# Performance work log

Hardware: AMD Instinct MI355X
Metric: run time of the kernel (lower is better)

## Reference

```python
import jax, jax.numpy as jnp
import numpy as np

MARGIN = 0.3
IN_FEATURES = 128
NUM_CLASSES = 100
BATCH = 4096


def setup_inputs() -> dict:
    key = jax.random.key(0)
    k1, k2, k3, k4 = jax.random.split(key, 4)
    embeddings = jax.random.normal(k1, (BATCH, IN_FEATURES), dtype=jnp.float32)
    labels = jax.random.randint(k2, (BATCH,), 0, NUM_CLASSES, dtype=jnp.int64)
    # nn.Linear params (kaiming-uniform-ish scale)
    bound = 1.0 / np.sqrt(IN_FEATURES)
    fc_w = jax.random.uniform(k3, (NUM_CLASSES, IN_FEATURES), jnp.float32, -bound, bound)
    fc_b = jax.random.uniform(k4, (NUM_CLASSES,), jnp.float32, -bound, bound)
    return {"embeddings": embeddings, "labels": labels, "fc_w": fc_w, "fc_b": fc_b}


def _triplet_hard(emb, labels, margin):
    # pairwise squared euclidean distances: ||a||^2 + ||b||^2 - 2 a.b
    sq = jnp.sum(emb * emb, axis=1)  # [B]
    d2 = sq[:, None] + sq[None, :] - 2.0 * (emb @ emb.T)
    dist = jnp.sqrt(jnp.clip(d2, 1e-12))  # [B, B]
    same = labels[:, None] == labels[None, :]  # [B, B] (diag True, as in torch)
    neg_inf = jnp.float32(-jnp.inf)
    pos_inf = jnp.float32(jnp.inf)
    ap = jnp.max(jnp.where(same, dist, neg_inf), axis=1)  # hardest positive
    an = jnp.min(jnp.where(same, pos_inf, dist), axis=1)  # hardest negative
    # MarginRankingLoss(target=1): mean(relu(-(an - ap) + margin))
    return jnp.mean(jax.nn.relu(ap - an + margin))


def _cross_entropy(logits, labels):
    logp = jax.nn.log_softmax(logits, axis=-1)
    return -jnp.mean(jnp.take_along_axis(logp, labels[:, None], axis=1)[:, 0])


def reference(embeddings, labels, fc_w, fc_b):
    logits = embeddings @ fc_w.T + fc_b  # [B, C]
    triplet = _triplet_hard(embeddings, labels, MARGIN)
    ce = _cross_entropy(logits, labels)
    return triplet + ce
```

## Files before the change

### kernel.cpp

```cpp
#include <hip/hip_runtime.h>
#include <math.h>

#define BATCH 4096
#define DIM 128
#define NCLS 100
#define MARGIN 0.3f
#define NTILE 544
#define GRID_MAIN 800

typedef __attribute__((ext_vector_type(8))) short short8;
typedef __attribute__((ext_vector_type(4))) float f32x4;

__device__ __forceinline__ unsigned short f2bf(float f) {
    unsigned int u = __float_as_uint(f);
    unsigned int r = (u + 0x7FFFu + ((u >> 16) & 1u)) >> 16;
    return (unsigned short)r;
}
__device__ __forceinline__ float bf2f(unsigned short b) {
    return __uint_as_float(((unsigned int)b) << 16);
}

#define ENC_MAX_ID 0x80000000u
#define ENC_MIN_ID 0x403FFFFFu
__device__ __forceinline__ unsigned int enc_max(float v) {
    return (__float_as_uint(v) >> 1) | 0x80000000u;
}
__device__ __forceinline__ float dec_max(unsigned int k) {
    return __uint_as_float((k & 0x7FFFFFFFu) << 1);
}
__device__ __forceinline__ unsigned int enc_min(float v) {
    return 0x7FFFFFFFu - (__float_as_uint(v) >> 1);
}
__device__ __forceinline__ float dec_min(unsigned int k) {
    return __uint_as_float((0x7FFFFFFFu - k) << 1);
}


__global__ __launch_bounds__(256) void prep_kernel(
        const float* __restrict__ emb, const float* __restrict__ fcw,
        unsigned short* __restrict__ ebf, float* __restrict__ sq,
        unsigned short* __restrict__ wbf, unsigned int* __restrict__ fanz) {
    int bid = blockIdx.x, tid = threadIdx.x;
    if (bid < 256) {
        int wave = tid >> 6, lane = tid & 63;
        unsigned int* dstg = reinterpret_cast<unsigned int*>(ebf) + bid * 1024;
        #pragma unroll
        for (int r = 0; r < 4; ++r) {
            int rowl = wave * 4 + r;
            int row = bid * 16 + rowl;
            const float2* src = reinterpret_cast<const float2*>(emb + row * DIM);
            float2 xy = src[lane];
            unsigned short b0 = f2bf(xy.x), b1 = f2bf(xy.y);
            float y0 = bf2f(b0), y1 = bf2f(b1);
            dstg[(lane >> 2) * 64 + rowl * 4 + (lane & 3)] =
                ((unsigned int)b1 << 16) | (unsigned int)b0;
            float acc = y0 * y0 + y1 * y1;
            #pragma unroll
            for (int off = 1; off < 64; off <<= 1) acc += __shfl_xor(acc, off, 64);
            if (lane == 0) sq[row] = acc;
        }
    } else {
        int idx = (bid - 256) * 256 + tid;
        for (int k = idx; k < 112 * DIM; k += 512) {
            int cls = k >> 7, d = k & 127;
            int dst = (cls >> 4) * 2048 + (d >> 3) * 128 + (cls & 15) * 8 + (d & 7);
            wbf[dst] = (k < NCLS * DIM) ? f2bf(fcw[k]) : (unsigned short)0;
        }
        for (int w = idx; w < 8194; w += 512)
            fanz[w] = 0;
    }
}

__global__ __launch_bounds__(256) void main_kernel(
        const unsigned short* __restrict__ ebf, const unsigned short* __restrict__ wbf,
        const float* __restrict__ sq, const int* __restrict__ labels,
        const float* __restrict__ fcb,
        unsigned int* __restrict__ maxk, unsigned int* __restrict__ mink,
        float* __restrict__ ce_sum, int* __restrict__ ticket,
        float* __restrict__ out) {
    __shared__ float lg[16][128];
    __shared__ unsigned int colk[512];
    __shared__ int lastFlag;
    int bid = blockIdx.x, tid = threadIdx.x;
    int wave = tid >> 6, lane = tid & 63;
    int lm = lane & 15, lq = lane >> 4;

    if (bid < NTILE) {
        int q = 0, rem = bid;
        while (rem >= 4 * (16 - q)) { rem -= 4 * (16 - q); ++q; }
        int cpr = 16 - q;
        int sub = rem / cpr, coff = rem % cpr;
        int rowgrp = 4 * q + sub;
        int chunk  = q + coff;

        int rbase = rowgrp * 64 + wave * 16;
        const unsigned short* apt = ebf + (rbase >> 4) * 2048 + lane * 8;
        short8 a0 = *reinterpret_cast<const short8*>(apt);
        short8 a1 = *reinterpret_cast<const short8*>(apt + 512);
        short8 a2 = *reinterpret_cast<const short8*>(apt + 1024);
        short8 a3 = *reinterpret_cast<const short8*>(apt + 1536);

        int labr[4];
        float sqr[4];
        #pragma unroll
        for (int r = 0; r < 4; ++r) {
            labr[r] = labels[rbase + lq * 4 + r];
            sqr[r]  = sq[rbase + lq * 4 + r];
        }

        colk[tid] = 0; colk[256 + tid] = 0;
        __syncthreads();

        float rmax[4] = {-INFINITY, -INFINITY, -INFINITY, -INFINITY};
        float rmin[4] = { INFINITY,  INFINITY,  INFINITY,  INFINITY};

        int cbase = chunk * 256;
        const unsigned short* bbase = ebf + (cbase >> 4) * 2048 + lane * 8;
        #pragma unroll 2
        for (int ct = 0; ct < 16; ++ct) {
            int col = cbase + ct * 16 + lm;
            const unsigned short* bp = bbase + ct * 2048;
            short8 b0 = *reinterpret_cast<const short8*>(bp);
            short8 b1 = *reinterpret_cast<const short8*>(bp + 512);
            short8 b2 = *reinterpret_cast<const short8*>(bp + 1024);
            short8 b3 = *reinterpret_cast<const short8*>(bp + 1536);
            f32x4 c = {0.f, 0.f, 0.f, 0.f};
            c = __builtin_amdgcn_mfma_f32_16x16x32_bf16(a0, b0, c, 0, 0, 0);
            c = __builtin_amdgcn_mfma_f32_16x16x32_bf16(a1, b1, c, 0, 0, 0);
            c = __builtin_amdgcn_mfma_f32_16x16x32_bf16(a2, b2, c, 0, 0, 0);
            c = __builtin_amdgcn_mfma_f32_16x16x32_bf16(a3, b3, c, 0, 0, 0);
            float sqc = sq[col];
            int lc = labels[col];
            float cmax = -INFINITY, cmin = INFINITY;
            #pragma unroll
            for (int r = 0; r < 4; ++r) {
                float v = fmaxf(fmaf(c[r], -2.0f, sqc) + sqr[r], 0.f);
                bool same = (lc == labr[r]);
                rmax[r] = same ? fmaxf(rmax[r], v) : rmax[r];
                rmin[r] = same ? rmin[r] : fminf(rmin[r], v);
                cmax    = same ? fmaxf(cmax, v) : cmax;
                cmin    = same ? cmin : fminf(cmin, v);
            }
            cmax = fmaxf(cmax, __shfl_xor(cmax, 16, 64));
            cmax = fmaxf(cmax, __shfl_xor(cmax, 32, 64));
            cmin = fminf(cmin, __shfl_xor(cmin, 16, 64));
            cmin = fminf(cmin, __shfl_xor(cmin, 32, 64));
            if (lq == 0) {
                atomicMax(&colk[ct * 16 + lm], enc_max(fmaxf(cmax, 0.f)));
                atomicMax(&colk[256 + ct * 16 + lm], enc_min(fmaxf(cmin, 0.f)));
            }
        }
        #pragma unroll
        for (int off = 1; off < 16; off <<= 1) {
            #pragma unroll
            for (int r = 0; r < 4; ++r) {
                rmax[r] = fmaxf(rmax[r], __shfl_xor(rmax[r], off, 64));
                rmin[r] = fminf(rmin[r], __shfl_xor(rmin[r], off, 64));
            }
        }
        if (lm == 0) {
            int row0 = rbase + lq * 4;
            #pragma unroll
            for (int r = 0; r < 4; ++r) {
                unsigned int kx = enc_max(fmaxf(rmax[r], 0.f));
                unsigned int kn = enc_min(fmaxf(rmin[r], 0.f));
                if (kx != ENC_MAX_ID)
                    __hip_atomic_fetch_max(&maxk[row0 + r], kx,
                                           __ATOMIC_RELAXED, __HIP_MEMORY_SCOPE_AGENT);
                if (kn != ENC_MIN_ID)
                    __hip_atomic_fetch_max(&mink[row0 + r], kn,
                                           __ATOMIC_RELAXED, __HIP_MEMORY_SCOPE_AGENT);
            }
        }
        __syncthreads();
        {
            unsigned int kx = colk[tid], kn = colk[256 + tid];
            int col = cbase + tid;
            if (kx > ENC_MAX_ID)
                __hip_atomic_fetch_max(&maxk[col], kx,
                                       __ATOMIC_RELAXED, __HIP_MEMORY_SCOPE_AGENT);
            if (kn != 0 && kn != ENC_MIN_ID)
                __hip_atomic_fetch_max(&mink[col], kn,
                                       __ATOMIC_RELAXED, __HIP_MEMORY_SCOPE_AGENT);
        }
    } else {
        int R0 = (bid - NTILE) * 16;
        lg[tid >> 4][112 + (tid & 15)] = -INFINITY;

        const unsigned short* apt = ebf + (R0 >> 4) * 2048 + lane * 8;
        short8 a0 = *reinterpret_cast<const short8*>(apt);
        short8 a1 = *reinterpret_cast<const short8*>(apt + 512);
        short8 a2 = *reinterpret_cast<const short8*>(apt + 1024);
        short8 a3 = *reinterpret_cast<const short8*>(apt + 1536);

        for (int t = wave * 2; t < 7 && t < wave * 2 + 2; ++t) {
            int cls = t * 16 + lm;
            const unsigned short* bp = wbf + t * 2048 + lane * 8;
            short8 b0 = *reinterpret_cast<const short8*>(bp);
            short8 b1 = *reinterpret_cast<const short8*>(bp + 512);
            short8 b2 = *reinterpret_cast<const short8*>(bp + 1024);
            short8 b3 = *reinterpret_cast<const short8*>(bp + 1536);
            f32x4 c = {0.f, 0.f, 0.f, 0.f};
            c = __builtin_amdgcn_mfma_f32_16x16x32_bf16(a0, b0, c, 0, 0, 0);
            c = __builtin_amdgcn_mfma_f32_16x16x32_bf16(a1, b1, c, 0, 0, 0);
            c = __builtin_amdgcn_mfma_f32_16x16x32_bf16(a2, b2, c, 0, 0, 0);
            c = __builtin_amdgcn_mfma_f32_16x16x32_bf16(a3, b3, c, 0, 0, 0);
            float bias = (cls < NCLS) ? fcb[cls] : -INFINITY;
            #pragma unroll
            for (int r = 0; r < 4; ++r)
                lg[lq * 4 + r][t * 16 + lm] = c[r] + bias;
        }
        __syncthreads();
        float cacc = 0.f;
        #pragma unroll
        for (int i = 0; i < 4; ++i) {
            int r = wave * 4 + i;
            float x0 = lg[r][lane], x1 = lg[r][lane + 64];
            float m = fmaxf(x0, x1);
            #pragma unroll
            for (int off = 1; off < 64; off <<= 1) m = fmaxf(m, __shfl_xor(m, off, 64));
            float s = expf(x0 - m) + expf(x1 - m);
            #pragma unroll
            for (int off = 1; off < 64; off <<= 1) s += __shfl_xor(s, off, 64);
            if (lane == 0) {
                int lab = labels[R0 + r];
                cacc += (m + logf(s)) - lg[r][lab];
            }
        }
        __syncthreads();
        if (lane == 0) lg[0][wave] = cacc;
        __syncthreads();
        if (tid == 0) {
            float bsum = lg[0][0] + lg[0][1] + lg[0][2] + lg[0][3];
            __hip_atomic_fetch_add(ce_sum, bsum,
                                   __ATOMIC_RELAXED, __HIP_MEMORY_SCOPE_AGENT);
        }
    }

    __syncthreads();
    asm volatile("s_waitcnt vmcnt(0)" ::: "memory");
    if (tid == 0) {
        int old = __hip_atomic_fetch_add(ticket, 1,
                                         __ATOMIC_RELAXED, __HIP_MEMORY_SCOPE_AGENT);
        lastFlag = (old == GRID_MAIN - 1);
    }
    __syncthreads();
    if (lastFlag) {
        float acc = 0.f;
        #pragma unroll
        for (int rr = 0; rr < 16; ++rr) {
            int row = rr * 256 + tid;
            unsigned int kx = __hip_atomic_load(&maxk[row], __ATOMIC_RELAXED,
                                                __HIP_MEMORY_SCOPE_AGENT);
            unsigned int kn = __hip_atomic_load(&mink[row], __ATOMIC_RELAXED,
                                                __HIP_MEMORY_SCOPE_AGENT);
            float ap = sqrtf(fmaxf(dec_max(kx), 1e-12f));
            float an = sqrtf(fmaxf(dec_min(kn), 1e-12f));
            acc += fmaxf(ap - an + MARGIN, 0.f);
        }
        float* red = reinterpret_cast<float*>(lg);
        red[tid] = acc;
        __syncthreads();
        for (int s = 128; s > 0; s >>= 1) {
            if (tid < s) red[tid] += red[tid + s];
            __syncthreads();
        }
        if (tid == 0) {
            float ces = __hip_atomic_load(ce_sum, __ATOMIC_RELAXED,
                                          __HIP_MEMORY_SCOPE_AGENT);
            out[0] = (red[0] + ces) * (1.0f / BATCH);
        }
    }
}

extern "C" void kernel_launch(void* const* d_in, const int* in_sizes, int n_in,
                              void* d_out, int out_size, void* d_ws, size_t ws_size,
                              hipStream_t stream) {
    const float* emb    = (const float*)d_in[0];
    const int*   labels = (const int*)  d_in[1];
    const float* fcw    = (const float*)d_in[2];
    const float* fcb    = (const float*)d_in[3];
    float* out = (float*)d_out;

    char* ws = (char*)d_ws;
    unsigned short* ebf = (unsigned short*)(ws);
    unsigned short* wbf = (unsigned short*)(ws + 1048576);
    float* sq           = (float*)(ws + 1081344);
    char* fan           = ws + 1097728;
    int*   ticket       = (int*)(fan);
    float* ce_sum       = (float*)(fan + 4);
    unsigned int* maxk  = (unsigned int*)(fan + 8);
    unsigned int* mink  = (unsigned int*)(fan + 8 + 16384);

    prep_kernel<<<258, 256, 0, stream>>>(emb, fcw, ebf, sq, wbf,
                                         (unsigned int*)fan);
    main_kernel<<<GRID_MAIN, 256, 0, stream>>>(ebf, wbf, sq, labels, fcb,
                                               maxk, mink, ce_sum, ticket, out);
}
```

Baseline: 95.37 us.

## Enlarge triplet tiles to 128 rows per block with two MFMA accumulators

Each distance-tile block now covers 128 rows (32 per wave, two 16-row MFMA groups) instead of 64, so every loaded B fragment feeds two MFMA chains. The triangular tile enumeration is remapped to match, which halves the tile block count and shrinks the grid. The aim is less global B-load traffic and fewer column-atomic flushes per unit of work, with more independent MFMAs in flight. The costs are higher register pressure, fewer blocks for occupancy, and dropping the unroll-2 pragma.

```diff
diff --git a/kernel.cpp b/kernel.cpp
--- a/kernel.cpp
+++ b/kernel.cpp
@@ -5,8 +5,8 @@
 #define DIM 128
 #define NCLS 100
 #define MARGIN 0.3f
-#define NTILE 544
-#define GRID_MAIN 800
+#define NTILE 272
+#define GRID_MAIN 528
 
 typedef __attribute__((ext_vector_type(8))) short short8;
 typedef __attribute__((ext_vector_type(4))) float f32x4;
@@ -86,37 +86,41 @@
     int lm = lane & 15, lq = lane >> 4;
 
     if (bid < NTILE) {
-        int q = 0, rem = bid;
-        while (rem >= 4 * (16 - q)) { rem -= 4 * (16 - q); ++q; }
-        int cpr = 16 - q;
-        int sub = rem / cpr, coff = rem % cpr;
-        int rowgrp = 4 * q + sub;
-        int chunk  = q + coff;
-
-        int rbase = rowgrp * 64 + wave * 16;
+        int c = 0, rem = bid;
+        while (rem >= 2 * c + 2) { rem -= 2 * c + 2; ++c; }
+        int rowgrp = rem;
+        int chunk  = c;
+
+        int rbase = rowgrp * 128 + wave * 32;
         const unsigned short* apt = ebf + (rbase >> 4) * 2048 + lane * 8;
         short8 a0 = *reinterpret_cast<const short8*>(apt);
         short8 a1 = *reinterpret_cast<const short8*>(apt + 512);
         short8 a2 = *reinterpret_cast<const short8*>(apt + 1024);
         short8 a3 = *reinterpret_cast<const short8*>(apt + 1536);
-
-        int labr[4];
-        float sqr[4];
-        #pragma unroll
-        for (int r = 0; r < 4; ++r) {
-            labr[r] = labels[rbase + lq * 4 + r];
-            sqr[r]  = sq[rbase + lq * 4 + r];
-        }
+        short8 a4 = *reinterpret_cast<const short8*>(apt + 2048);
+        short8 a5 = *reinterpret_cast<const short8*>(apt + 2560);
+        short8 a6 = *reinterpret_cast<const short8*>(apt + 3072);
+        short8 a7 = *reinterpret_cast<const short8*>(apt + 3584);
+
+        int labr[8];
+        float sqr[8];
+        #pragma unroll
+        for (int g = 0; g < 2; ++g)
+            #pragma unroll
+            for (int r = 0; r < 4; ++r) {
+                labr[g * 4 + r] = labels[rbase + g * 16 + lq * 4 + r];
+                sqr[g * 4 + r]  = sq[rbase + g * 16 + lq * 4 + r];
+            }
 
         colk[tid] = 0; colk[256 + tid] = 0;
         __syncthreads();
 
-        float rmax[4] = {-INFINITY, -INFINITY, -INFINITY, -INFINITY};
-        float rmin[4] = { INFINITY,  INFINITY,  INFINITY,  INFINITY};
+        float rmax[8], rmin[8];
+        #pragma unroll
+        for (int r = 0; r < 8; ++r) { rmax[r] = -INFINITY; rmin[r] = INFINITY; }
 
         int cbase = chunk * 256;
         const unsigned short* bbase = ebf + (cbase >> 4) * 2048 + lane * 8;
-        #pragma unroll 2
         for (int ct = 0; ct < 16; ++ct) {
             int col = cbase + ct * 16 + lm;
             const unsigned short* bp = bbase + ct * 2048;
@@ -124,22 +128,33 @@
             short8 b1 = *reinterpret_cast<const short8*>(bp + 512);
             short8 b2 = *reinterpret_cast<const short8*>(bp + 1024);
             short8 b3 = *reinterpret_cast<const short8*>(bp + 1536);
-            f32x4 c = {0.f, 0.f, 0.f, 0.f};
-            c = __builtin_amdgcn_mfma_f32_16x16x32_bf16(a0, b0, c, 0, 0, 0);
-            c = __builtin_amdgcn_mfma_f32_16x16x32_bf16(a1, b1, c, 0, 0, 0);
-            c = __builtin_amdgcn_mfma_f32_16x16x32_bf16(a2, b2, c, 0, 0, 0);
-            c = __builtin_amdgcn_mfma_f32_16x16x32_bf16(a3, b3, c, 0, 0, 0);
+            f32x4 c0 = {0.f, 0.f, 0.f, 0.f};
+            f32x4 c1 = {0.f, 0.f, 0.f, 0.f};
+            c0 = __builtin_amdgcn_mfma_f32_16x16x32_bf16(a0, b0, c0, 0, 0, 0);
+            c1 = __builtin_amdgcn_mfma_f32_16x16x32_bf16(a4, b0, c1, 0, 0, 0);
+            c0 = __builtin_amdgcn_mfma_f32_16x16x32_bf16(a1, b1, c0, 0, 0, 0);
+            c1 = __builtin_amdgcn_mfma_f32_16x16x32_bf16(a5, b1, c1, 0, 0, 0);
+            c0 = __builtin_amdgcn_mfma_f32_16x16x32_bf16(a2, b2, c0, 0, 0, 0);
+            c1 = __builtin_amdgcn_mfma_f32_16x16x32_bf16(a6, b2, c1, 0, 0, 0);
+            c0 = __builtin_amdgcn_mfma_f32_16x16x32_bf16(a3, b3, c0, 0, 0, 0);
+            c1 = __builtin_amdgcn_mfma_f32_16x16x32_bf16(a7, b3, c1, 0, 0, 0);
             float sqc = sq[col];
             int lc = labels[col];
             float cmax = -INFINITY, cmin = INFINITY;
             #pragma unroll
             for (int r = 0; r < 4; ++r) {
-                float v = fmaxf(fmaf(c[r], -2.0f, sqc) + sqr[r], 0.f);
-                bool same = (lc == labr[r]);
-                rmax[r] = same ? fmaxf(rmax[r], v) : rmax[r];
-                rmin[r] = same ? rmin[r] : fminf(rmin[r], v);
-                cmax    = same ? fmaxf(cmax, v) : cmax;
-                cmin    = same ? cmin : fminf(cmin, v);
+                float v0 = fmaxf(fmaf(c0[r], -2.0f, sqc) + sqr[r], 0.f);
+                bool s0 = (lc == labr[r]);
+                rmax[r] = s0 ? fmaxf(rmax[r], v0) : rmax[r];
+                rmin[r] = s0 ? rmin[r] : fminf(rmin[r], v0);
+                cmax    = s0 ? fmaxf(cmax, v0) : cmax;
+                cmin    = s0 ? cmin : fminf(cmin, v0);
+                float v1 = fmaxf(fmaf(c1[r], -2.0f, sqc) + sqr[4 + r], 0.f);
+                bool s1 = (lc == labr[4 + r]);
+                rmax[4 + r] = s1 ? fmaxf(rmax[4 + r], v1) : rmax[4 + r];
+                rmin[4 + r] = s1 ? rmin[4 + r] : fminf(rmin[4 + r], v1);
+                cmax        = s1 ? fmaxf(cmax, v1) : cmax;
+                cmin        = s1 ? cmin : fminf(cmin, v1);
             }
             cmax = fmaxf(cmax, __shfl_xor(cmax, 16, 64));
             cmax = fmaxf(cmax, __shfl_xor(cmax, 32, 64));
@@ -153,24 +168,26 @@
         #pragma unroll
         for (int off = 1; off < 16; off <<= 1) {
             #pragma unroll
-            for (int r = 0; r < 4; ++r) {
+            for (int r = 0; r < 8; ++r) {
                 rmax[r] = fmaxf(rmax[r], __shfl_xor(rmax[r], off, 64));
                 rmin[r] = fminf(rmin[r], __shfl_xor(rmin[r], off, 64));
             }
         }
         if (lm == 0) {
-            int row0 = rbase + lq * 4;
-            #pragma unroll
-            for (int r = 0; r < 4; ++r) {
-                unsigned int kx = enc_max(fmaxf(rmax[r], 0.f));
-                unsigned int kn = enc_min(fmaxf(rmin[r], 0.f));
-                if (kx != ENC_MAX_ID)
-                    __hip_atomic_fetch_max(&maxk[row0 + r], kx,
-                                           __ATOMIC_RELAXED, __HIP_MEMORY_SCOPE_AGENT);
-                if (kn != ENC_MIN_ID)
-                    __hip_atomic_fetch_max(&mink[row0 + r], kn,
-                                           __ATOMIC_RELAXED, __HIP_MEMORY_SCOPE_AGENT);
-            }
+            #pragma unroll
+            for (int g = 0; g < 2; ++g)
+                #pragma unroll
+                for (int r = 0; r < 4; ++r) {
+                    int row = rbase + g * 16 + lq * 4 + r;
+                    unsigned int kx = enc_max(fmaxf(rmax[g * 4 + r], 0.f));
+                    unsigned int kn = enc_min(fmaxf(rmin[g * 4 + r], 0.f));
+                    if (kx != ENC_MAX_ID)
+                        __hip_atomic_fetch_max(&maxk[row], kx,
+                                               __ATOMIC_RELAXED, __HIP_MEMORY_SCOPE_AGENT);
+                    if (kn != ENC_MIN_ID)
+                        __hip_atomic_fetch_max(&mink[row], kn,
+                                               __ATOMIC_RELAXED, __HIP_MEMORY_SCOPE_AGENT);
+                }
         }
         __syncthreads();
         {
```

Measured after the change: 94.11 us. No clear change (-1.3%).
